# Kernel tuning notes

Measured on AMD Instinct MI355X. Metric: run time of the kernel, lower is better.

## Reference

```python
import jax, jax.numpy as jnp
import numpy as np

D_MODEL, D_INT, H = 1024, 64, 16
LAMBDA_INIT = 0.8
B, S = 2, 2048
LN_EPS = 1e-5


def setup_inputs() -> dict:
    key = jax.random.key(0)
    ks = jax.random.split(key, 12)
    sd = 0.02
    return {
        "x": jax.random.normal(ks[0], (B, S, D_MODEL), dtype=jnp.float32),
        "lambda_current": jnp.float32(0.5),
        "mask": jnp.ones((B, S), dtype=jnp.int32),
        # stacked per-head params (WQ1/WK1/WV; WQ2/WK2 are unused in source due to bug)
        "wq": sd * jax.random.normal(ks[1], (H, D_MODEL, D_INT), dtype=jnp.float32),
        "bq": sd * jax.random.normal(ks[2], (H, D_INT), dtype=jnp.float32),
        "wk": sd * jax.random.normal(ks[3], (H, D_MODEL, D_INT), dtype=jnp.float32),
        "bk": sd * jax.random.normal(ks[4], (H, D_INT), dtype=jnp.float32),
        "wv": sd * jax.random.normal(ks[5], (H, D_MODEL, 2 * D_INT), dtype=jnp.float32),
        "bv": sd * jax.random.normal(ks[6], (H, 2 * D_INT), dtype=jnp.float32),
        "wo": sd * jax.random.normal(ks[7], (2 * H * D_INT, D_MODEL), dtype=jnp.float32),
        "bo": sd * jax.random.normal(ks[8], (D_MODEL,), dtype=jnp.float32),
        "ln_g": jnp.ones((2 * D_INT,), dtype=jnp.float32),
        "ln_b": jnp.zeros((2 * D_INT,), dtype=jnp.float32),
    }


def reference(x, lambda_current, mask, wq, bq, wk, bk, wv, bv, wo, bo, ln_g, ln_b):
    b, s, d_model = x.shape
    scale = 1.0 / (d_model ** 0.5)  # source divides by sqrt(WQ1.in_features)
    # per-head projections: [H, B, S, d]
    Q = jnp.einsum('bsd,hdk->hbsk', x, wq) + bq[:, None, None, :]
    K = jnp.einsum('bsd,hdk->hbsk', x, wk) + bk[:, None, None, :]
    V = jnp.einsum('bsd,hdv->hbsv', x, wv) + bv[:, None, None, :]
    scores = jnp.einsum('hbsk,hbtk->hbst', Q, K) * scale
    scores = jnp.where(mask[None, :, None, :] == 0, -jnp.inf, scores)
    A1 = jax.nn.softmax(scores, axis=-1)
    # source bug: Q2/K2 reuse WQ1/WK1 => A2 == A1, so A = A1 - lambda*A2 = (1-lambda)*A1
    A = (1.0 - lambda_current) * A1
    out = jnp.einsum('hbst,hbtv->hbsv', A, V)  # [H,B,S,2*D_INT]
    # per-head LayerNorm (shared gamma/beta), then scale by (1 - lambda_init)
    mu = out.mean(-1, keepdims=True)
    var = out.var(-1, keepdims=True)
    out = (out - mu) / jnp.sqrt(var + LN_EPS) * ln_g + ln_b
    out = out * (1.0 - LAMBDA_INIT)
    cat = out.transpose(1, 2, 0, 3).reshape(b, s, -1)  # concat heads on feature dim
    res = cat @ wo + bo
    return (res, A)
```

## Files before the change

### kernel.cpp

```cpp
#include <hip/hip_runtime.h>
#include <hip/hip_bf16.h>

#define DM   1024
#define DI   64
#define H_   16
#define B_   2
#define S_   2048
#define NTOK 4096

typedef unsigned short u16;
typedef unsigned int u32;
typedef __attribute__((ext_vector_type(8))) short s16x8;
typedef __attribute__((ext_vector_type(4))) float f32x4;
typedef __attribute__((ext_vector_type(4))) unsigned int u32x4;
typedef __attribute__((ext_vector_type(4))) unsigned short u16x4;

#define AS1 __attribute__((address_space(1)))
#define AS3 __attribute__((address_space(3)))

static __device__ __forceinline__ u16 f2bf(float f) {
  unsigned int u = __builtin_bit_cast(unsigned int, f);
  unsigned int r = (u + 0x7fffu + ((u >> 16) & 1u)) >> 16;
  return (u16)r;
}

static __device__ __forceinline__ void gload_lds16(const u16* g, u16* l) {
  __builtin_amdgcn_global_load_lds((const AS1 u32*)(const void*)g,
                                   (AS3 u32*)(void*)l, 16, 0, 0);
}

static __device__ __forceinline__ void lds_barrier() {
  asm volatile("s_waitcnt lgkmcnt(0)\n\ts_barrier" ::: "memory");
}


__global__ void k_cvt_x(const float* __restrict__ in, u16* __restrict__ out) {
  int i = (blockIdx.x * 256 + threadIdx.x) * 4;
  float4 v = *(const float4*)&in[i];
  u16x4 o;
  o[0] = f2bf(v.x); o[1] = f2bf(v.y); o[2] = f2bf(v.z); o[3] = f2bf(v.w);
  *(u16x4*)&out[i] = o;
}

__global__ void k_small(const float* __restrict__ bq, const float* __restrict__ bk,
                        const float* __restrict__ bv, const int* __restrict__ mask,
                        float* __restrict__ bc, float* __restrict__ mbias) {
  int t = blockIdx.x * 256 + threadIdx.x;
  if (t < 1024) bc[t] = bq[t];
  else if (t < 2048) bc[t] = bk[t - 1024];
  else if (t < 4096) bc[t] = bv[t - 2048];
  else if (t < 8192) { int i = t - 4096; mbias[i] = mask[i] ? 0.f : -1e38f; }
}

__global__ void k_tr_f2b(const float* __restrict__ in, u16* __restrict__ out, int R, int C) {
  __shared__ float t[32][33];
  const float* src = in + (size_t)blockIdx.z * R * C;
  u16* dst = out + (size_t)blockIdx.z * C * R;
  int r0 = blockIdx.y * 32, c0 = blockIdx.x * 32;
  for (int i = threadIdx.y; i < 32; i += 8)
    t[i][threadIdx.x] = src[(size_t)(r0 + i) * C + c0 + threadIdx.x];
  __syncthreads();
  for (int i = threadIdx.y; i < 32; i += 8)
    dst[(size_t)(c0 + i) * R + r0 + threadIdx.x] = f2bf(t[threadIdx.x][i]);
}

__global__ void k_tr_b2b(const u16* __restrict__ in, u16* __restrict__ out, int R, int C) {
  __shared__ u16 t[32][33];
  const u16* src = in + (size_t)blockIdx.z * R * C;
  u16* dst = out + (size_t)blockIdx.z * C * R;
  int r0 = blockIdx.y * 32, c0 = blockIdx.x * 32;
  for (int i = threadIdx.y; i < 32; i += 8)
    t[i][threadIdx.x] = src[(size_t)(r0 + i) * C + c0 + threadIdx.x];
  __syncthreads();
  for (int i = threadIdx.y; i < 32; i += 8)
    dst[(size_t)(c0 + i) * R + r0 + threadIdx.x] = t[threadIdx.x][i];
}

template<int MODE>
__global__ __launch_bounds__(256)
void k_gemm(const u16* __restrict__ A, const u16* __restrict__ Bt,
            const float* __restrict__ bias, int Kdim,
            u16* __restrict__ q_out, u16* __restrict__ k_out, u16* __restrict__ v_out,
            float* __restrict__ res_out) {
  const int tid = threadIdx.x;
  const int l = tid & 63, w = tid >> 6;
  const int wm = w >> 1, wn = w & 1;
  const int g = l >> 4, lo = l & 15;
  const int m0 = blockIdx.y * 128, n0 = blockIdx.x * 128;
  __shared__ u16 As[128 * 64];
  __shared__ u16 Bs[128 * 64];
  f32x4 acc[4][4] = {};
  for (int kt = 0; kt < Kdim; kt += 64) {
    __syncthreads();
    for (int cid = tid; cid < 1024; cid += 256) {
      int r = cid >> 3, c = (cid & 7) * 8;
      gload_lds16(&A[(size_t)(m0 + r) * Kdim + kt + c], &As[cid * 8]);
      gload_lds16(&Bt[(size_t)(n0 + r) * Kdim + kt + c], &Bs[cid * 8]);
    }
    __syncthreads();
    for (int kc = 0; kc < 64; kc += 32) {
      s16x8 a[4], b[4];
      for (int i = 0; i < 4; i++)
        a[i] = *(const s16x8*)&As[(wm * 64 + i * 16 + lo) * 64 + kc + 8 * g];
      for (int i = 0; i < 4; i++)
        b[i] = *(const s16x8*)&Bs[(wn * 64 + i * 16 + lo) * 64 + kc + 8 * g];
      for (int mi = 0; mi < 4; mi++)
        for (int ni = 0; ni < 4; ni++)
          acc[mi][ni] = __builtin_amdgcn_mfma_f32_16x16x32_bf16(a[mi], b[ni], acc[mi][ni], 0, 0, 0);
    }
  }
  for (int mi = 0; mi < 4; mi++)
    for (int ni = 0; ni < 4; ni++)
      for (int j = 0; j < 4; j++) {
        int m = m0 + wm * 64 + mi * 16 + g * 4 + j;
        int n = n0 + wn * 64 + ni * 16 + lo;
        float v = acc[mi][ni][j] + bias[n];
        if (MODE == 0) {
          int bb = m >> 11, s = m & 2047;
          if (n < 1024) {
            int h = n >> 6, d = n & 63;
            q_out[(((size_t)h * B_ + bb) * S_ + s) * 64 + d] = f2bf(v);
          } else if (n < 2048) {
            int nn = n - 1024; int h = nn >> 6, d = nn & 63;
            k_out[(((size_t)h * B_ + bb) * S_ + s) * 64 + d] = f2bf(v);
          } else {
            int nn = n - 2048; int h = nn >> 7, d = nn & 127;
            v_out[(((size_t)h * B_ + bb) * S_ + s) * 128 + d] = f2bf(v);
          }
        } else {
          res_out[(size_t)m * 1024 + n] = v;
        }
      }
}

__global__ __launch_bounds__(256, 4)
void k_attn(const u16* __restrict__ Qb, const u16* __restrict__ Kb,
            const u16* __restrict__ Vtb, const float* __restrict__ mbias,
            const float* __restrict__ lam_p, const float* __restrict__ ln_g,
            const float* __restrict__ ln_b, float* __restrict__ A_out,
            u16* __restrict__ cat) {
  const int tid = threadIdx.x, l = tid & 63, w = tid >> 6;
  const int g = l >> 4, lo = l & 15;
  const int bid = blockIdx.x;
  const int xcd = bid & 7, idx = bid >> 3;
  const int hb = xcd * 4 + (idx >> 5);
  const int s0 = (idx & 31) * 64;
  const int b = hb & 1, h = hb >> 1;
  const float scale2 = 0.03125f * 1.44269504f;
  const float pfac = 1.0f - lam_p[0];

  __shared__ __align__(16) u16 Ks[64 * 72];
  __shared__ __align__(16) u16 Vs[128 * 72];
  __shared__ __align__(16) u16 Ps[4][16 * 72];

  const u16* Qhb = Qb + (size_t)hb * S_ * 64;
  const u16* Khb = Kb + (size_t)hb * S_ * 64;
  const u16* Vthb = Vtb + (size_t)hb * 128 * S_;
  const float* mb = mbias + (size_t)b * S_;

  const int q = s0 + w * 16 + lo;
  const s16x8 q0 = *(const s16x8*)&Qhb[(size_t)q * 64 + 8 * g];
  const s16x8 q1 = *(const s16x8*)&Qhb[(size_t)q * 64 + 32 + 8 * g];
  float* Arow = A_out + ((size_t)hb * S_ + q) * S_;

  const int kr = tid >> 3, kc8 = (tid & 7) * 8;

  {
    *(u32x4*)&Ks[kr * 72 + kc8] = *(const u32x4*)&Khb[(size_t)kr * 64 + kc8];
    int cid = tid + 256; int r = cid >> 3, c = (cid & 7) * 8;
    *(u32x4*)&Ks[r * 72 + c] = *(const u32x4*)&Khb[(size_t)r * 64 + c];
  }
  __syncthreads();
  f32x4 psv = {};
  for (int t = 0; t < 32; t++) {
    const u16* rbuf = (t & 1) ? Vs : Ks;
    u16* wbuf = (t & 1) ? Ks : Vs;
    const int kt = t * 64;
    const int ktn = (kt + 64) & (S_ - 1);
    u32x4 kreg0 = *(const u32x4*)&Khb[(size_t)(ktn + kr) * 64 + kc8];
    u32x4 kreg1 = *(const u32x4*)&Khb[(size_t)(ktn + kr + 32) * 64 + kc8];
#pragma unroll
    for (int nf = 0; nf < 4; nf++) {
      s16x8 k0 = *(const s16x8*)&rbuf[(nf * 16 + lo) * 72 + 8 * g];
      s16x8 k1 = *(const s16x8*)&rbuf[(nf * 16 + lo) * 72 + 32 + 8 * g];
      f32x4 z = {};
      z = __builtin_amdgcn_mfma_f32_16x16x32_bf16(k0, q0, z, 0, 0, 0);
      z = __builtin_amdgcn_mfma_f32_16x16x32_bf16(k1, q1, z, 0, 0, 0);
      f32x4 m4 = *(const f32x4*)&mb[kt + nf * 16 + g * 4];
      psv[0] += __builtin_exp2f(z[0] * scale2 + m4[0]);
      psv[1] += __builtin_exp2f(z[1] * scale2 + m4[1]);
      psv[2] += __builtin_exp2f(z[2] * scale2 + m4[2]);
      psv[3] += __builtin_exp2f(z[3] * scale2 + m4[3]);
    }
    *(u32x4*)&wbuf[kr * 72 + kc8] = kreg0;
    *(u32x4*)&wbuf[(kr + 32) * 72 + kc8] = kreg1;
    __syncthreads();
  }
  float ps = (psv[0] + psv[1]) + (psv[2] + psv[3]);
  ps += __shfl_xor(ps, 16, 64);
  ps += __shfl_xor(ps, 32, 64);
  const float rinv = pfac / ps;

#pragma unroll
  for (int i = 0; i < 4; i++) {
    int cid = tid + i * 256;
    int r = cid >> 3, c = (cid & 7) * 8;
    *(u32x4*)&Vs[r * 72 + c] = *(const u32x4*)&Vthb[(size_t)r * S_ + c];
  }
  __syncthreads();

  f32x4 o[8] = {};
  for (int t = 0; t < 32; t++) {
    const int kt = t * 64;
    const bool pre = (t < 31);
    u32x4 kreg0, kreg1, vreg[4];
    if (pre) {
      const int ktn = kt + 64;
      kreg0 = *(const u32x4*)&Khb[(size_t)(ktn + kr) * 64 + kc8];
      kreg1 = *(const u32x4*)&Khb[(size_t)(ktn + kr + 32) * 64 + kc8];
#pragma unroll
      for (int i = 0; i < 4; i++) {
        int cid = tid + i * 256;
        vreg[i] = *(const u32x4*)&Vthb[(size_t)(cid >> 3) * S_ + ktn + (cid & 7) * 8];
      }
    }
    f32x4 z[4];
#pragma unroll
    for (int nf = 0; nf < 4; nf++) {
      s16x8 k0 = *(const s16x8*)&Ks[(nf * 16 + lo) * 72 + 8 * g];
      s16x8 k1 = *(const s16x8*)&Ks[(nf * 16 + lo) * 72 + 32 + 8 * g];
      f32x4 zz = {};
      zz = __builtin_amdgcn_mfma_f32_16x16x32_bf16(k0, q0, zz, 0, 0, 0);
      z[nf] = __builtin_amdgcn_mfma_f32_16x16x32_bf16(k1, q1, zz, 0, 0, 0);
    }
#pragma unroll
    for (int nf = 0; nf < 4; nf++) {
      f32x4 m4 = *(const f32x4*)&mb[kt + nf * 16 + g * 4];
      f32x4 p4;
      p4[0] = __builtin_exp2f(z[nf][0] * scale2 + m4[0]) * rinv;
      p4[1] = __builtin_exp2f(z[nf][1] * scale2 + m4[1]) * rinv;
      p4[2] = __builtin_exp2f(z[nf][2] * scale2 + m4[2]) * rinv;
      p4[3] = __builtin_exp2f(z[nf][3] * scale2 + m4[3]) * rinv;
      __builtin_nontemporal_store(p4, (f32x4*)&Arow[kt + nf * 16 + g * 4]);
      u16x4 pb;
      pb[0] = f2bf(p4[0]); pb[1] = f2bf(p4[1]);
      pb[2] = f2bf(p4[2]); pb[3] = f2bf(p4[3]);
      *(u16x4*)&Ps[w][lo * 72 + nf * 16 + g * 4] = pb;
    }
#pragma unroll
    for (int kc = 0; kc < 2; kc++) {
      s16x8 pa = *(const s16x8*)&Ps[w][lo * 72 + kc * 32 + 8 * g];
#pragma unroll
      for (int vf = 0; vf < 8; vf++) {
        s16x8 bv = *(const s16x8*)&Vs[(vf * 16 + lo) * 72 + kc * 32 + 8 * g];
        o[vf] = __builtin_amdgcn_mfma_f32_16x16x32_bf16(pa, bv, o[vf], 0, 0, 0);
      }
    }
    lds_barrier();
    if (pre) {
      *(u32x4*)&Ks[kr * 72 + kc8] = kreg0;
      *(u32x4*)&Ks[(kr + 32) * 72 + kc8] = kreg1;
#pragma unroll
      for (int i = 0; i < 4; i++) {
        int cid = tid + i * 256;
        *(u32x4*)&Vs[(cid >> 3) * 72 + (cid & 7) * 8] = vreg[i];
      }
    }
    lds_barrier();
  }

#pragma unroll
  for (int j = 0; j < 4; j++) {
    float sum = 0.f, sq = 0.f;
#pragma unroll
    for (int vf = 0; vf < 8; vf++) { float xv = o[vf][j]; sum += xv; sq += xv * xv; }
    for (int msk = 1; msk < 16; msk <<= 1) {
      sum += __shfl_xor(sum, msk, 64);
      sq += __shfl_xor(sq, msk, 64);
    }
    float mean = sum * (1.f / 128.f);
    float var = sq * (1.f / 128.f) - mean * mean;
    float rstd = rsqrtf(var + 1e-5f);
    int s = s0 + w * 16 + g * 4 + j;
    u16* cp = cat + ((size_t)(b * S_ + s)) * 2048 + h * 128;
#pragma unroll
    for (int vf = 0; vf < 8; vf++) {
      int c = vf * 16 + lo;
      float y = (o[vf][j] - mean) * rstd * ln_g[c] + ln_b[c];
      cp[c] = f2bf(y * 0.2f);
    }
  }
}


extern "C" void kernel_launch(void* const* d_in, const int* in_sizes, int n_in,
                              void* d_out, int out_size, void* d_ws, size_t ws_size,
                              hipStream_t stream) {
  const float* x    = (const float*)d_in[0];
  const float* lam  = (const float*)d_in[1];
  const int*   mask = (const int*)d_in[2];
  const float* wq   = (const float*)d_in[3];
  const float* bq   = (const float*)d_in[4];
  const float* wk   = (const float*)d_in[5];
  const float* bk   = (const float*)d_in[6];
  const float* wv   = (const float*)d_in[7];
  const float* bv   = (const float*)d_in[8];
  const float* wo   = (const float*)d_in[9];
  const float* bo   = (const float*)d_in[10];
  const float* lng  = (const float*)d_in[11];
  const float* lnb  = (const float*)d_in[12];

  float* res = (float*)d_out;
  float* A   = res + (size_t)NTOK * DM;

  char* ws = (char*)d_ws;
  size_t off = 0;
  auto alloc = [&](size_t bytes) {
    void* p = ws + off;
    off += (bytes + 255) & ~(size_t)255;
    return p;
  };
  u16*   xb    = (u16*)  alloc((size_t)NTOK * DM * 2);
  u16*   Wct   = (u16*)  alloc((size_t)4096 * 1024 * 2);
  float* bc    = (float*)alloc(4096 * 4);
  float* mbias = (float*)alloc(4096 * 4);
  u16*   wot   = (u16*)  alloc((size_t)1024 * 2048 * 2);
  u16*   Qb    = (u16*)  alloc((size_t)32 * S_ * 64 * 2);
  u16*   Kb2   = (u16*)  alloc((size_t)32 * S_ * 64 * 2);
  u16*   Vb    = (u16*)  alloc((size_t)32 * S_ * 128 * 2);
  u16*   Vtb   = (u16*)  alloc((size_t)32 * S_ * 128 * 2);
  u16*   catb  = (u16*)ws;

  k_cvt_x<<<4096, 256, 0, stream>>>(x, xb);
  k_small<<<32, 256, 0, stream>>>(bq, bk, bv, mask, bc, mbias);
  k_tr_f2b<<<dim3(2, 32, 16), dim3(32, 8), 0, stream>>>(wq, Wct, 1024, 64);
  k_tr_f2b<<<dim3(2, 32, 16), dim3(32, 8), 0, stream>>>(wk, Wct + 1024 * 1024, 1024, 64);
  k_tr_f2b<<<dim3(4, 32, 16), dim3(32, 8), 0, stream>>>(wv, Wct + 2048 * 1024, 1024, 128);
  k_tr_f2b<<<dim3(32, 64, 1), dim3(32, 8), 0, stream>>>(wo, wot, 2048, 1024);
  k_gemm<0><<<dim3(32, 32), 256, 0, stream>>>(xb, Wct, bc, 1024, Qb, Kb2, Vb, nullptr);
  k_tr_b2b<<<dim3(4, 64, 32), dim3(32, 8), 0, stream>>>(Vb, Vtb, 2048, 128);
  k_attn<<<dim3(1024), 256, 0, stream>>>(Qb, Kb2, Vtb, mbias, lam, lng, lnb, A, catb);
  k_gemm<1><<<dim3(8, 32), 256, 0, stream>>>(catb, wot, bo, 2048, nullptr, nullptr, nullptr, res);
}
```

Measured before the change: 348.5 us.

## Compute V transposed via swapped GEMM, add tile mask skip, smaller output GEMM tiles

The V projection now runs as a separate GEMM with weights as the A operand and x as B, writing V directly in transposed layout. This removes the separate bf16 transpose kernel and its intermediate buffer. A per-64-key-tile mask bitmap lets attention skip loading the mask bias for tiles with no masked keys. The output projection uses a 64x128 tile GEMM to launch more blocks. The transposed-V epilogue writes strided bf16 values, which may coalesce poorly.

New measurement: 349.8 us. About the same (+0.4%).

```diff
diff --git a/kernel.cpp b/kernel.cpp
--- a/kernel.cpp
+++ b/kernel.cpp
@@ -44,12 +44,21 @@
 
 __global__ void k_small(const float* __restrict__ bq, const float* __restrict__ bk,
                         const float* __restrict__ bv, const int* __restrict__ mask,
-                        float* __restrict__ bc, float* __restrict__ mbias) {
+                        float* __restrict__ bc, float* __restrict__ mbias,
+                        u32* __restrict__ tmask) {
   int t = blockIdx.x * 256 + threadIdx.x;
   if (t < 1024) bc[t] = bq[t];
   else if (t < 2048) bc[t] = bk[t - 1024];
   else if (t < 4096) bc[t] = bv[t - 2048];
   else if (t < 8192) { int i = t - 4096; mbias[i] = mask[i] ? 0.f : -1e38f; }
+  else if (t < 8256) {
+    int tt = t - 8192;
+    const int* mp = mask + (tt >> 5) * S_ + (tt & 31) * 64;
+    int any0 = 0;
+    for (int i = 0; i < 64; i++) any0 |= (mp[i] == 0);
+    unsigned long long bal = __ballot(any0);
+    if (tt == 0) { tmask[0] = (u32)bal; tmask[1] = (u32)(bal >> 32); }
+  }
 }
 
 __global__ void k_tr_f2b(const float* __restrict__ in, u16* __restrict__ out, int R, int C) {
@@ -64,24 +73,11 @@
     dst[(size_t)(c0 + i) * R + r0 + threadIdx.x] = f2bf(t[threadIdx.x][i]);
 }
 
-__global__ void k_tr_b2b(const u16* __restrict__ in, u16* __restrict__ out, int R, int C) {
-  __shared__ u16 t[32][33];
-  const u16* src = in + (size_t)blockIdx.z * R * C;
-  u16* dst = out + (size_t)blockIdx.z * C * R;
-  int r0 = blockIdx.y * 32, c0 = blockIdx.x * 32;
-  for (int i = threadIdx.y; i < 32; i += 8)
-    t[i][threadIdx.x] = src[(size_t)(r0 + i) * C + c0 + threadIdx.x];
-  __syncthreads();
-  for (int i = threadIdx.y; i < 32; i += 8)
-    dst[(size_t)(c0 + i) * R + r0 + threadIdx.x] = t[threadIdx.x][i];
-}
-
 template<int MODE>
 __global__ __launch_bounds__(256)
 void k_gemm(const u16* __restrict__ A, const u16* __restrict__ Bt,
             const float* __restrict__ bias, int Kdim,
-            u16* __restrict__ q_out, u16* __restrict__ k_out, u16* __restrict__ v_out,
-            float* __restrict__ res_out) {
+            u16* __restrict__ q_out, u16* __restrict__ k_out, u16* __restrict__ vt_out) {
   const int tid = threadIdx.x;
   const int l = tid & 63, w = tid >> 6;
   const int wm = w >> 1, wn = w & 1;
@@ -114,31 +110,73 @@
       for (int j = 0; j < 4; j++) {
         int m = m0 + wm * 64 + mi * 16 + g * 4 + j;
         int n = n0 + wn * 64 + ni * 16 + lo;
-        float v = acc[mi][ni][j] + bias[n];
         if (MODE == 0) {
+          float v = acc[mi][ni][j] + bias[n];
           int bb = m >> 11, s = m & 2047;
           if (n < 1024) {
             int h = n >> 6, d = n & 63;
             q_out[(((size_t)h * B_ + bb) * S_ + s) * 64 + d] = f2bf(v);
-          } else if (n < 2048) {
+          } else {
             int nn = n - 1024; int h = nn >> 6, d = nn & 63;
             k_out[(((size_t)h * B_ + bb) * S_ + s) * 64 + d] = f2bf(v);
-          } else {
-            int nn = n - 2048; int h = nn >> 7, d = nn & 127;
-            v_out[(((size_t)h * B_ + bb) * S_ + s) * 128 + d] = f2bf(v);
           }
         } else {
-          res_out[(size_t)m * 1024 + n] = v;
+          float v = acc[mi][ni][j] + bias[m];
+          int h = m >> 7, d = m & 127;
+          int bb = n >> 11, s = n & 2047;
+          vt_out[(((size_t)h * B_ + bb) * 128 + d) * S_ + s] = f2bf(v);
         }
+      }
+}
+
+__global__ __launch_bounds__(256)
+void k_gemm64(const u16* __restrict__ A, const u16* __restrict__ Bt,
+              const float* __restrict__ bias, int Kdim, float* __restrict__ res_out) {
+  const int tid = threadIdx.x;
+  const int l = tid & 63, w = tid >> 6;
+  const int wm = w >> 1, wn = w & 1;
+  const int g = l >> 4, lo = l & 15;
+  const int m0 = blockIdx.y * 64, n0 = blockIdx.x * 128;
+  __shared__ u16 As[64 * 64];
+  __shared__ u16 Bs[128 * 64];
+  f32x4 acc[2][4] = {};
+  for (int kt = 0; kt < Kdim; kt += 64) {
+    __syncthreads();
+    for (int cid = tid; cid < 512; cid += 256) {
+      int r = cid >> 3, c = (cid & 7) * 8;
+      gload_lds16(&A[(size_t)(m0 + r) * Kdim + kt + c], &As[cid * 8]);
+    }
+    for (int cid = tid; cid < 1024; cid += 256) {
+      int r = cid >> 3, c = (cid & 7) * 8;
+      gload_lds16(&Bt[(size_t)(n0 + r) * Kdim + kt + c], &Bs[cid * 8]);
+    }
+    __syncthreads();
+    for (int kc = 0; kc < 64; kc += 32) {
+      s16x8 a[2], b[4];
+      for (int i = 0; i < 2; i++)
+        a[i] = *(const s16x8*)&As[(wm * 32 + i * 16 + lo) * 64 + kc + 8 * g];
+      for (int i = 0; i < 4; i++)
+        b[i] = *(const s16x8*)&Bs[(wn * 64 + i * 16 + lo) * 64 + kc + 8 * g];
+      for (int mi = 0; mi < 2; mi++)
+        for (int ni = 0; ni < 4; ni++)
+          acc[mi][ni] = __builtin_amdgcn_mfma_f32_16x16x32_bf16(a[mi], b[ni], acc[mi][ni], 0, 0, 0);
+    }
+  }
+  for (int mi = 0; mi < 2; mi++)
+    for (int ni = 0; ni < 4; ni++)
+      for (int j = 0; j < 4; j++) {
+        int m = m0 + wm * 32 + mi * 16 + g * 4 + j;
+        int n = n0 + wn * 64 + ni * 16 + lo;
+        res_out[(size_t)m * 1024 + n] = acc[mi][ni][j] + bias[n];
       }
 }
 
 __global__ __launch_bounds__(256, 4)
 void k_attn(const u16* __restrict__ Qb, const u16* __restrict__ Kb,
             const u16* __restrict__ Vtb, const float* __restrict__ mbias,
-            const float* __restrict__ lam_p, const float* __restrict__ ln_g,
-            const float* __restrict__ ln_b, float* __restrict__ A_out,
-            u16* __restrict__ cat) {
+            const u32* __restrict__ tmask, const float* __restrict__ lam_p,
+            const float* __restrict__ ln_g, const float* __restrict__ ln_b,
+            float* __restrict__ A_out, u16* __restrict__ cat) {
   const int tid = threadIdx.x, l = tid & 63, w = tid >> 6;
   const int g = l >> 4, lo = l & 15;
   const int bid = blockIdx.x;
@@ -148,6 +186,7 @@
   const int b = hb & 1, h = hb >> 1;
   const float scale2 = 0.03125f * 1.44269504f;
   const float pfac = 1.0f - lam_p[0];
+  const u32 tm = tmask[b];
 
   __shared__ __align__(16) u16 Ks[64 * 72];
   __shared__ __align__(16) u16 Vs[128 * 72];
@@ -177,6 +216,7 @@
     u16* wbuf = (t & 1) ? Ks : Vs;
     const int kt = t * 64;
     const int ktn = (kt + 64) & (S_ - 1);
+    const bool mskt = (tm >> t) & 1;
     u32x4 kreg0 = *(const u32x4*)&Khb[(size_t)(ktn + kr) * 64 + kc8];
     u32x4 kreg1 = *(const u32x4*)&Khb[(size_t)(ktn + kr + 32) * 64 + kc8];
 #pragma unroll
@@ -186,7 +226,8 @@
       f32x4 z = {};
       z = __builtin_amdgcn_mfma_f32_16x16x32_bf16(k0, q0, z, 0, 0, 0);
       z = __builtin_amdgcn_mfma_f32_16x16x32_bf16(k1, q1, z, 0, 0, 0);
-      f32x4 m4 = *(const f32x4*)&mb[kt + nf * 16 + g * 4];
+      f32x4 m4 = {};
+      if (mskt) m4 = *(const f32x4*)&mb[kt + nf * 16 + g * 4];
       psv[0] += __builtin_exp2f(z[0] * scale2 + m4[0]);
       psv[1] += __builtin_exp2f(z[1] * scale2 + m4[1]);
       psv[2] += __builtin_exp2f(z[2] * scale2 + m4[2]);
@@ -213,6 +254,7 @@
   for (int t = 0; t < 32; t++) {
     const int kt = t * 64;
     const bool pre = (t < 31);
+    const bool mskt = (tm >> t) & 1;
     u32x4 kreg0, kreg1, vreg[4];
     if (pre) {
       const int ktn = kt + 64;
@@ -235,7 +277,8 @@
     }
 #pragma unroll
     for (int nf = 0; nf < 4; nf++) {
-      f32x4 m4 = *(const f32x4*)&mb[kt + nf * 16 + g * 4];
+      f32x4 m4 = {};
+      if (mskt) m4 = *(const f32x4*)&mb[kt + nf * 16 + g * 4];
       f32x4 p4;
       p4[0] = __builtin_exp2f(z[nf][0] * scale2 + m4[0]) * rinv;
       p4[1] = __builtin_exp2f(z[nf][1] * scale2 + m4[1]) * rinv;
@@ -324,21 +367,22 @@
   u16*   Wct   = (u16*)  alloc((size_t)4096 * 1024 * 2);
   float* bc    = (float*)alloc(4096 * 4);
   float* mbias = (float*)alloc(4096 * 4);
+  u32*   tmask = (u32*)  alloc(2 * 4);
   u16*   wot   = (u16*)  alloc((size_t)1024 * 2048 * 2);
   u16*   Qb    = (u16*)  alloc((size_t)32 * S_ * 64 * 2);
   u16*   Kb2   = (u16*)  alloc((size_t)32 * S_ * 64 * 2);
-  u16*   Vb    = (u16*)  alloc((size_t)32 * S_ * 128 * 2);
   u16*   Vtb   = (u16*)  alloc((size_t)32 * S_ * 128 * 2);
   u16*   catb  = (u16*)ws;
 
   k_cvt_x<<<4096, 256, 0, stream>>>(x, xb);
-  k_small<<<32, 256, 0, stream>>>(bq, bk, bv, mask, bc, mbias);
+  k_small<<<33, 256, 0, stream>>>(bq, bk, bv, mask, bc, mbias, tmask);
   k_tr_f2b<<<dim3(2, 32, 16), dim3(32, 8), 0, stream>>>(wq, Wct, 1024, 64);
   k_tr_f2b<<<dim3(2, 32, 16), dim3(32, 8), 0, stream>>>(wk, Wct + 1024 * 1024, 1024, 64);
   k_tr_f2b<<<dim3(4, 32, 16), dim3(32, 8), 0, stream>>>(wv, Wct + 2048 * 1024, 1024, 128);
   k_tr_f2b<<<dim3(32, 64, 1), dim3(32, 8), 0, stream>>>(wo, wot, 2048, 1024);
-  k_gemm<0><<<dim3(32, 32), 256, 0, stream>>>(xb, Wct, bc, 1024, Qb, Kb2, Vb, nullptr);
-  k_tr_b2b<<<dim3(4, 64, 32), dim3(32, 8), 0, stream>>>(Vb, Vtb, 2048, 128);
-  k_attn<<<dim3(1024), 256, 0, stream>>>(Qb, Kb2, Vtb, mbias, lam, lng, lnb, A, catb);
-  k_gemm<1><<<dim3(8, 32), 256, 0, stream>>>(catb, wot, bo, 2048, nullptr, nullptr, nullptr, res);
-}
+  k_gemm<0><<<dim3(16, 32), 256, 0, stream>>>(xb, Wct, bc, 1024, Qb, Kb2, nullptr);
+  k_gemm<2><<<dim3(32, 16), 256, 0, stream>>>(Wct + (size_t)2048 * 1024, xb, bc + 2048,
+                                              1024, nullptr, nullptr, Vtb);
+  k_attn<<<dim3(1024), 256, 0, stream>>>(Qb, Kb2, Vtb, mbias, tmask, lam, lng, lnb, A, catb);
+  k_gemm64<<<dim3(8, 64), 256, 0, stream>>>(catb, wot, bo, 2048, res);
+}
```
